# Kernel optimization log

Measured on AMD Instinct MI355X. Metric: run time of the kernel, lower is better.

Reference implementation:

```python
import jax, jax.numpy as jnp
import numpy as np

LAMBDA = 0.7
RATIO = 3
EPS = 1e-6


def setup_inputs() -> dict:
    key = jax.random.key(0)
    k1, k2, k3 = jax.random.split(key, 3)
    bs, n, w, h = 8, 7, 640, 640
    preds = jax.random.normal(k1, (bs, n, w, h), dtype=jnp.float32)
    labels = jax.random.randint(k2, (bs, n, w, h), 0, 2, dtype=jnp.int32)
    training_mask = jax.random.randint(k3, (bs, w, h), 0, 2, dtype=jnp.int32)
    return {"preds": preds, "labels": labels, "training_mask": training_mask}


def _dice(S, G):
    # S, G: [C, P]; per-channel dice coefficient, then mean over channels
    num = 2.0 * jnp.sum(S * G, axis=-1)
    den = jnp.sum(S * S, axis=-1) + jnp.sum(G * G, axis=-1) + EPS
    return jnp.mean(num / den)


def _single_sample(pred, label, mask):
    # pred, label: [n, P]; mask: [P]
    P = pred.shape[-1]
    p = jax.nn.sigmoid(pred)
    pred_n = p[-1] * mask            # masked full-text prediction
    label_n = label[-1] * mask

    # --- OHEM mask M (cal_M): keep all positives + top (ratio*n_pos) hardest negatives ---
    pos = pred_n >= 0.5
    n_pos = jnp.sum(pos)
    n_neg_all = jnp.sum(~pos)
    k = n_pos * RATIO
    # sigmoid outputs are in (0,1); sentinel -1 pushes positives to the end of the descending sort
    neg_vals = jnp.where(pos, -1.0, pred_n)
    sorted_desc = -jnp.sort(-neg_vals)
    thr = sorted_desc[jnp.clip(k - 1, 0, P - 1)]  # k-th largest negative score
    ohem_active = (n_neg_all > k) & (k > 0)
    M = jnp.where(ohem_active, (pred_n >= thr).astype(jnp.float32), 1.0)

    # L_c: dice loss on OHEM-selected full-text map
    L_c = 1.0 - _dice((pred_n * M)[None, :], (label_n * M)[None, :])

    # L_s: dice loss on shrunk kernels, gated by predicted text region W
    W = (pred_n >= 0.5).astype(jnp.float32)
    L_s = 1.0 - _dice(p[:-1] * W, label[:-1] * W)

    loss = LAMBDA * L_c + (1.0 - LAMBDA) * L_s
    return L_c, L_s, loss


def reference(preds, labels, training_mask):
    bs, n, w, h = preds.shape
    preds = preds.reshape(bs, n, w * h)
    labels = labels.reshape(bs, n, w * h).astype(jnp.float32)
    mask = training_mask.reshape(bs, w * h).astype(jnp.float32)
    L_c, L_s, loss = jax.vmap(_single_sample)(preds, labels, mask)
    # reduction='mean'
    return L_c.mean(), L_s.mean(), loss.mean()
```

## Files before the change

### kernel.cpp

```cpp
#include <hip/hip_runtime.h>

#define BS   8
#define NCH  7
#define PX   409600
#define NBIN 65536
#define NCHK 256
#define WIN_LO 0x3000u
#define WIN_SZ 4096
#define EPSF 1e-6f

__device__ __forceinline__ float sigf(float x) {
    return 1.0f / (1.0f + __expf(-x));
}

__device__ __forceinline__ unsigned wred_u(unsigned v) {
    #pragma unroll
    for (int o = 32; o; o >>= 1) v += __shfl_down(v, o);
    return v;
}

__device__ __forceinline__ float wred_f(float v) {
    #pragma unroll
    for (int o = 32; o; o >>= 1) v += __shfl_down(v, o);
    return v;
}

__global__ __launch_bounds__(256) void k_main(const float* __restrict__ preds,
                                              const int* __restrict__ labels,
                                              const int* __restrict__ mask,
                                              unsigned* __restrict__ hist1,
                                              unsigned* __restrict__ chunks1,
                                              unsigned* __restrict__ n_pos,
                                              float* __restrict__ sums) {
    int b = blockIdx.y;
    const float* pr = preds + (size_t)b * NCH * PX;
    const int*   lb = labels + (size_t)b * NCH * PX;
    const int*   mk = mask + (size_t)b * PX;

    __shared__ unsigned lh[WIN_SZ];
    for (int j = threadIdx.x; j < WIN_SZ; j += 256) lh[j] = 0u;
    __syncthreads();

    unsigned pos_cnt = 0, zero_cnt = 0;
    float acc[18];
    #pragma unroll
    for (int j = 0; j < 18; j++) acc[j] = 0.f;

    for (int g = blockIdx.x * 256 + threadIdx.x; g < PX / 4; g += gridDim.x * 256) {
        int px = g * 4;
        float4 p6 = *(const float4*)(pr + 6 * PX + px);
        int4   m4 = *(const int4*)(mk + px);
        float mm[4]  = {(float)m4.x, (float)m4.y, (float)m4.z, (float)m4.w};
        float p6a[4] = {p6.x, p6.y, p6.z, p6.w};
        float W[4];
        #pragma unroll
        for (int u = 0; u < 4; u++) {
            float pn = sigf(p6a[u]) * mm[u];
            if (pn >= 0.5f) {
                pos_cnt++; W[u] = 1.0f;
            } else {
                W[u] = 0.0f;
                unsigned bits = __float_as_uint(pn);
                if (bits == 0u) {
                    zero_cnt++;
                } else {
                    unsigned hb = bits >> 16;
                    if (hb - WIN_LO < WIN_SZ) {
                        atomicAdd(&lh[hb - WIN_LO], 1u);
                    } else {
                        atomicAdd(&hist1[(size_t)b * NBIN + hb], 1u);
                        atomicAdd(&chunks1[b * NCHK + (hb >> 8)], 1u);
                    }
                }
            }
        }
        #pragma unroll
        for (int c = 0; c < 6; c++) {
            float4 pc4 = *(const float4*)(pr + c * PX + px);
            int4   lc4 = *(const int4*)(lb + c * PX + px);
            float pcs[4] = {pc4.x, pc4.y, pc4.z, pc4.w};
            float lcs[4] = {(float)lc4.x, (float)lc4.y, (float)lc4.z, (float)lc4.w};
            #pragma unroll
            for (int u = 0; u < 4; u++) {
                float s = sigf(pcs[u]);
                float l = lcs[u];
                acc[c]      += s * l * W[u];
                acc[6 + c]  += s * s * W[u];
                acc[12 + c] += l * W[u];
            }
        }
    }
    __syncthreads();

    for (int j = threadIdx.x; j < WIN_SZ; j += 256) {
        unsigned c = lh[j];
        if (c) atomicAdd(&hist1[(size_t)b * NBIN + WIN_LO + j], c);
    }
    __shared__ unsigned csum[256];
    {
        unsigned s = 0;
        int chunk = threadIdx.x >> 4, part = threadIdx.x & 15;
        const unsigned* base = &lh[chunk * 256 + part * 16];
        #pragma unroll
        for (int j = 0; j < 16; j++) s += base[j];
        csum[threadIdx.x] = s;
    }
    __syncthreads();
    if (threadIdx.x < 16) {
        unsigned s = 0;
        #pragma unroll
        for (int j = 0; j < 16; j++) s += csum[threadIdx.x * 16 + j];
        if (s) atomicAdd(&chunks1[b * NCHK + 48 + threadIdx.x], s);
    }

    __shared__ unsigned ws2[2][4];
    unsigned pv = wred_u(pos_cnt), zv = wred_u(zero_cnt);
    int lane = threadIdx.x & 63, wid = threadIdx.x >> 6;
    if (lane == 0) { ws2[0][wid] = pv; ws2[1][wid] = zv; }
    __syncthreads();
    if (threadIdx.x == 0) {
        unsigned pt = 0, zt = 0;
        #pragma unroll
        for (int w = 0; w < 4; w++) { pt += ws2[0][w]; zt += ws2[1][w]; }
        if (pt) atomicAdd(&n_pos[b], pt);
        if (zt) {
            atomicAdd(&hist1[(size_t)b * NBIN], zt);
            atomicAdd(&chunks1[b * NCHK], zt);
        }
    }

    __shared__ float red[4][18];
    #pragma unroll
    for (int j = 0; j < 18; j++) {
        float v = wred_f(acc[j]);
        if (lane == 0) red[wid][j] = v;
    }
    __syncthreads();
    if (threadIdx.x < 18) {
        float tot = red[0][threadIdx.x] + red[1][threadIdx.x] +
                    red[2][threadIdx.x] + red[3][threadIdx.x];
        atomicAdd(&sums[b * 21 + 3 + threadIdx.x], tot);
    }
}

__device__ void select2(const unsigned* __restrict__ chunks,
                        const unsigned* __restrict__ bins,
                        unsigned k, unsigned* out_bin, unsigned* out_rank) {
    __shared__ unsigned cs[256];
    __shared__ unsigned sel_c, sel_r;
    int t = threadIdx.x;
    cs[t] = chunks[t];
    __syncthreads();
    #pragma unroll
    for (int off = 1; off < 256; off <<= 1) {
        unsigned v = cs[t];
        unsigned a = (t + off < 256) ? cs[t + off] : 0u;
        __syncthreads();
        cs[t] = v + a;
        __syncthreads();
    }
    {
        unsigned sfx  = cs[t];
        unsigned sfx1 = (t < 255) ? cs[t + 1] : 0u;
        if (sfx >= k && sfx1 < k) { sel_c = (unsigned)t; sel_r = k - sfx1; }
    }
    __syncthreads();
    unsigned chunk = sel_c, krem = sel_r;
    cs[t] = bins[chunk * 256 + t];
    __syncthreads();
    #pragma unroll
    for (int off = 1; off < 256; off <<= 1) {
        unsigned v = cs[t];
        unsigned a = (t + off < 256) ? cs[t + off] : 0u;
        __syncthreads();
        cs[t] = v + a;
        __syncthreads();
    }
    {
        unsigned sfx  = cs[t];
        unsigned sfx1 = (t < 255) ? cs[t + 1] : 0u;
        if (sfx >= krem && sfx1 < krem) {
            *out_bin  = chunk * 256 + (unsigned)t;
            *out_rank = krem - sfx1;
        }
    }
    __syncthreads();
}

__global__ __launch_bounds__(256) void k_find_hi(const unsigned* __restrict__ hist1,
                                                 const unsigned* __restrict__ chunks1,
                                                 const unsigned* __restrict__ n_pos,
                                                 unsigned* __restrict__ hi_bin,
                                                 unsigned* __restrict__ rankv,
                                                 unsigned* __restrict__ activev,
                                                 float* __restrict__ thr) {
    int b = blockIdx.x;
    unsigned np_ = n_pos[b];
    unsigned k = np_ * 3u;
    unsigned nneg = (unsigned)PX - np_;
    if (!(nneg > k && k > 0u)) {
        if (threadIdx.x == 0) { activev[b] = 0u; thr[b] = -1.0f; }
        return;
    }
    __shared__ unsigned rb, rr;
    select2(chunks1 + b * NCHK, hist1 + (size_t)b * NBIN, k, &rb, &rr);
    if (threadIdx.x == 0) {
        activev[b] = 1u;
        hi_bin[b] = rb;
        rankv[b] = rr;
        if (rb == 0u) thr[b] = 0.0f;
    }
}

__global__ __launch_bounds__(256) void k_refine(const float* __restrict__ preds,
                                                const int* __restrict__ mask,
                                                const unsigned* __restrict__ hi_bin,
                                                const unsigned* __restrict__ activev,
                                                unsigned* __restrict__ hist2,
                                                unsigned* __restrict__ chunks2) {
    int b = blockIdx.y;
    if (!activev[b]) return;
    unsigned hi = hi_bin[b];
    if (hi == 0u) return;
    const float* pr = preds + ((size_t)b * NCH + 6) * PX;
    const int* mk = mask + (size_t)b * PX;
    unsigned* h2 = hist2 + (size_t)b * NBIN;
    unsigned* c2 = chunks2 + b * NCHK;
    for (int g = blockIdx.x * 256 + threadIdx.x; g < PX / 4; g += gridDim.x * 256) {
        int px = g * 4;
        float4 p6 = *(const float4*)(pr + px);
        int4   m4 = *(const int4*)(mk + px);
        float p6a[4] = {p6.x, p6.y, p6.z, p6.w};
        float mm[4]  = {(float)m4.x, (float)m4.y, (float)m4.z, (float)m4.w};
        #pragma unroll
        for (int u = 0; u < 4; u++) {
            float pn = sigf(p6a[u]) * mm[u];
            if (pn < 0.5f) {
                unsigned bits = __float_as_uint(pn);
                if ((bits >> 16) == hi) {
                    unsigned lo = bits & 0xFFFFu;
                    atomicAdd(&h2[lo], 1u);
                    atomicAdd(&c2[lo >> 8], 1u);
                }
            }
        }
    }
}

__global__ __launch_bounds__(256) void k_find_lo(const unsigned* __restrict__ hist2,
                                                 const unsigned* __restrict__ chunks2,
                                                 const unsigned* __restrict__ hi_bin,
                                                 const unsigned* __restrict__ rankv,
                                                 const unsigned* __restrict__ activev,
                                                 float* __restrict__ thr) {
    int b = blockIdx.x;
    if (!activev[b]) return;
    unsigned hi = hi_bin[b];
    if (hi == 0u) return;
    __shared__ unsigned rb, rr;
    select2(chunks2 + b * NCHK, hist2 + (size_t)b * NBIN, rankv[b], &rb, &rr);
    if (threadIdx.x == 0) thr[b] = __uint_as_float((hi << 16) | rb);
}

__global__ __launch_bounds__(256) void k_lc(const float* __restrict__ preds,
                                            const int* __restrict__ labels,
                                            const int* __restrict__ mask,
                                            const float* __restrict__ thr,
                                            float* __restrict__ sums) {
    int b = blockIdx.y;
    const float* pr = preds + ((size_t)b * NCH + 6) * PX;
    const int*   lb = labels + ((size_t)b * NCH + 6) * PX;
    const int*   mk = mask + (size_t)b * PX;
    float thr_b = thr[b];

    float a0 = 0.f, a1 = 0.f, a2 = 0.f;
    for (int g = blockIdx.x * 256 + threadIdx.x; g < PX / 4; g += gridDim.x * 256) {
        int px = g * 4;
        float4 p6 = *(const float4*)(pr + px);
        int4   l4 = *(const int4*)(lb + px);
        int4   m4 = *(const int4*)(mk + px);
        float p6a[4] = {p6.x, p6.y, p6.z, p6.w};
        float la[4]  = {(float)l4.x, (float)l4.y, (float)l4.z, (float)l4.w};
        float mm[4]  = {(float)m4.x, (float)m4.y, (float)m4.z, (float)m4.w};
        #pragma unroll
        for (int u = 0; u < 4; u++) {
            float pn = sigf(p6a[u]) * mm[u];
            float Mi = (pn >= thr_b) ? 1.0f : 0.0f;
            float ln = la[u] * mm[u];
            a0 += pn * ln * Mi;
            a1 += pn * pn * Mi;
            a2 += ln * Mi;
        }
    }
    __shared__ float red[4][3];
    int lane = threadIdx.x & 63, wid = threadIdx.x >> 6;
    float v0 = wred_f(a0), v1 = wred_f(a1), v2 = wred_f(a2);
    if (lane == 0) { red[wid][0] = v0; red[wid][1] = v1; red[wid][2] = v2; }
    __syncthreads();
    if (threadIdx.x < 3) {
        float tot = red[0][threadIdx.x] + red[1][threadIdx.x] +
                    red[2][threadIdx.x] + red[3][threadIdx.x];
        atomicAdd(&sums[b * 21 + threadIdx.x], tot);
    }
}

__global__ void k_final(const float* __restrict__ sums, float* __restrict__ out) {
    int t = threadIdx.x;
    float Lc = 0.f, Ls = 0.f;
    if (t < BS) {
        const float* s = sums + t * 21;
        Lc = 1.0f - (2.0f * s[0]) / (s[1] + s[2] + EPSF);
        float acc = 0.f;
        #pragma unroll
        for (int c = 0; c < 6; c++)
            acc += (2.0f * s[3 + c]) / (s[9 + c] + s[15 + c] + EPSF);
        Ls = 1.0f - acc * (1.0f / 6.0f);
    }
    #pragma unroll
    for (int o = 4; o; o >>= 1) { Lc += __shfl_down(Lc, o); Ls += __shfl_down(Ls, o); }
    if (t == 0) {
        float lc_m = Lc * (1.0f / (float)BS);
        float ls_m = Ls * (1.0f / (float)BS);
        out[0] = lc_m;
        out[1] = ls_m;
        out[2] = 0.7f * lc_m + 0.3f * ls_m;
    }
}

extern "C" void kernel_launch(void* const* d_in, const int* in_sizes, int n_in,
                              void* d_out, int out_size, void* d_ws, size_t ws_size,
                              hipStream_t stream) {
    const float* preds = (const float*)d_in[0];
    const int* labels  = (const int*)d_in[1];
    const int* mask    = (const int*)d_in[2];
    float* out = (float*)d_out;

    unsigned* hist1   = (unsigned*)d_ws;
    unsigned* hist2   = hist1 + (size_t)BS * NBIN;
    unsigned* chunks1 = hist2 + (size_t)BS * NBIN;
    unsigned* chunks2 = chunks1 + (size_t)BS * NCHK;
    unsigned* n_pos   = chunks2 + (size_t)BS * NCHK;
    unsigned* hi_bin  = n_pos + BS;
    unsigned* rankv   = hi_bin + BS;
    unsigned* activev = rankv + BS;
    float*    thr     = (float*)(activev + BS);
    float*    sums    = thr + BS;

    size_t zero_words = (size_t)2 * BS * NBIN + (size_t)2 * BS * NCHK + 5 * BS + (size_t)BS * 21;
    hipMemsetAsync(d_ws, 0, zero_words * sizeof(unsigned), stream);

    hipLaunchKernelGGL(k_main, dim3(100, BS), dim3(256), 0, stream,
                       preds, labels, mask, hist1, chunks1, n_pos, sums);

    hipLaunchKernelGGL(k_find_hi, dim3(BS), dim3(256), 0, stream,
                       hist1, chunks1, n_pos, hi_bin, rankv, activev, thr);

    hipLaunchKernelGGL(k_refine, dim3(32, BS), dim3(256), 0, stream,
                       preds, mask, hi_bin, activev, hist2, chunks2);

    hipLaunchKernelGGL(k_find_lo, dim3(BS), dim3(256), 0, stream,
                       hist2, chunks2, hi_bin, rankv, activev, thr);

    hipLaunchKernelGGL(k_lc, dim3(100, BS), dim3(256), 0, stream,
                       preds, labels, mask, thr, sums);

    hipLaunchKernelGGL(k_final, dim3(1), dim3(64), 0, stream, sums, out);
}
```

Measured before the change: 233.0 us.

## Use one-pass-per-thread grids, drop shared window histogram and chunk counters

The main, refine and Lc kernels now launch 400 blocks per sample so each thread handles exactly one float4 group with all loads issued up front, replacing the grid-stride loops over 100 or 32 blocks. The shared-memory window histogram and the separate chunk-count arrays are removed. Every non-positive value goes straight to a global histogram atomic, and select2 now builds its chunk sums by reducing the histogram itself. Float atomics on the sums are replaced by per-block partial writes that k_final reduces, which shrinks the memset. The changes target latency hiding and bookkeeping overhead, but they add heavy global atomic contention on hot histogram bins, since many values fall into a few bins.

```diff
diff --git a/kernel.cpp b/kernel.cpp
--- a/kernel.cpp
+++ b/kernel.cpp
@@ -4,9 +4,7 @@
 #define NCH  7
 #define PX   409600
 #define NBIN 65536
-#define NCHK 256
-#define WIN_LO 0x3000u
-#define WIN_SZ 4096
+#define NBLK 400
 #define EPSF 1e-6f
 
 __device__ __forceinline__ float sigf(float x) {
@@ -25,131 +23,100 @@
     return v;
 }
 
-__global__ __launch_bounds__(256) void k_main(const float* __restrict__ preds,
-                                              const int* __restrict__ labels,
-                                              const int* __restrict__ mask,
-                                              unsigned* __restrict__ hist1,
-                                              unsigned* __restrict__ chunks1,
-                                              unsigned* __restrict__ n_pos,
-                                              float* __restrict__ sums) {
+__global__ __launch_bounds__(256, 4) void k_main(const float* __restrict__ preds,
+                                                 const int* __restrict__ labels,
+                                                 const int* __restrict__ mask,
+                                                 unsigned* __restrict__ hist1,
+                                                 unsigned* __restrict__ n_pos,
+                                                 float* __restrict__ part) {
     int b = blockIdx.y;
+    int bx = blockIdx.x;
+    int px = (bx * 256 + threadIdx.x) * 4;
     const float* pr = preds + (size_t)b * NCH * PX;
     const int*   lb = labels + (size_t)b * NCH * PX;
     const int*   mk = mask + (size_t)b * PX;
 
-    __shared__ unsigned lh[WIN_SZ];
-    for (int j = threadIdx.x; j < WIN_SZ; j += 256) lh[j] = 0u;
-    __syncthreads();
-
+    float4 p6 = *(const float4*)(pr + 6 * PX + px);
+    int4   m4 = *(const int4*)(mk + px);
+    float4 pc[6];
+    int4   lc[6];
+    #pragma unroll
+    for (int c = 0; c < 6; c++) {
+        pc[c] = *(const float4*)(pr + c * PX + px);
+        lc[c] = *(const int4*)(lb + c * PX + px);
+    }
+
+    float mm[4]  = {(float)m4.x, (float)m4.y, (float)m4.z, (float)m4.w};
+    float p6a[4] = {p6.x, p6.y, p6.z, p6.w};
+    float W[4];
     unsigned pos_cnt = 0, zero_cnt = 0;
+    unsigned* hb = hist1 + (size_t)b * NBIN;
+
+    #pragma unroll
+    for (int u = 0; u < 4; u++) {
+        float pn = sigf(p6a[u]) * mm[u];
+        if (pn >= 0.5f) {
+            pos_cnt++; W[u] = 1.0f;
+        } else {
+            W[u] = 0.0f;
+            unsigned bits = __float_as_uint(pn);
+            if (bits == 0u) zero_cnt++;
+            else            atomicAdd(&hb[bits >> 16], 1u);
+        }
+    }
+
     float acc[18];
     #pragma unroll
     for (int j = 0; j < 18; j++) acc[j] = 0.f;
-
-    for (int g = blockIdx.x * 256 + threadIdx.x; g < PX / 4; g += gridDim.x * 256) {
-        int px = g * 4;
-        float4 p6 = *(const float4*)(pr + 6 * PX + px);
-        int4   m4 = *(const int4*)(mk + px);
-        float mm[4]  = {(float)m4.x, (float)m4.y, (float)m4.z, (float)m4.w};
-        float p6a[4] = {p6.x, p6.y, p6.z, p6.w};
-        float W[4];
+    #pragma unroll
+    for (int c = 0; c < 6; c++) {
+        float pcs[4] = {pc[c].x, pc[c].y, pc[c].z, pc[c].w};
+        float lcs[4] = {(float)lc[c].x, (float)lc[c].y, (float)lc[c].z, (float)lc[c].w};
         #pragma unroll
         for (int u = 0; u < 4; u++) {
-            float pn = sigf(p6a[u]) * mm[u];
-            if (pn >= 0.5f) {
-                pos_cnt++; W[u] = 1.0f;
-            } else {
-                W[u] = 0.0f;
-                unsigned bits = __float_as_uint(pn);
-                if (bits == 0u) {
-                    zero_cnt++;
-                } else {
-                    unsigned hb = bits >> 16;
-                    if (hb - WIN_LO < WIN_SZ) {
-                        atomicAdd(&lh[hb - WIN_LO], 1u);
-                    } else {
-                        atomicAdd(&hist1[(size_t)b * NBIN + hb], 1u);
-                        atomicAdd(&chunks1[b * NCHK + (hb >> 8)], 1u);
-                    }
-                }
-            }
-        }
-        #pragma unroll
-        for (int c = 0; c < 6; c++) {
-            float4 pc4 = *(const float4*)(pr + c * PX + px);
-            int4   lc4 = *(const int4*)(lb + c * PX + px);
-            float pcs[4] = {pc4.x, pc4.y, pc4.z, pc4.w};
-            float lcs[4] = {(float)lc4.x, (float)lc4.y, (float)lc4.z, (float)lc4.w};
-            #pragma unroll
-            for (int u = 0; u < 4; u++) {
-                float s = sigf(pcs[u]);
-                float l = lcs[u];
-                acc[c]      += s * l * W[u];
-                acc[6 + c]  += s * s * W[u];
-                acc[12 + c] += l * W[u];
-            }
-        }
-    }
-    __syncthreads();
-
-    for (int j = threadIdx.x; j < WIN_SZ; j += 256) {
-        unsigned c = lh[j];
-        if (c) atomicAdd(&hist1[(size_t)b * NBIN + WIN_LO + j], c);
-    }
-    __shared__ unsigned csum[256];
-    {
-        unsigned s = 0;
-        int chunk = threadIdx.x >> 4, part = threadIdx.x & 15;
-        const unsigned* base = &lh[chunk * 256 + part * 16];
-        #pragma unroll
-        for (int j = 0; j < 16; j++) s += base[j];
-        csum[threadIdx.x] = s;
-    }
-    __syncthreads();
-    if (threadIdx.x < 16) {
-        unsigned s = 0;
-        #pragma unroll
-        for (int j = 0; j < 16; j++) s += csum[threadIdx.x * 16 + j];
-        if (s) atomicAdd(&chunks1[b * NCHK + 48 + threadIdx.x], s);
-    }
-
+            float s = sigf(pcs[u]);
+            float l = lcs[u];
+            acc[c]      += s * l * W[u];
+            acc[6 + c]  += s * s * W[u];
+            acc[12 + c] += l * W[u];
+        }
+    }
+
+    int lane = threadIdx.x & 63, wid = threadIdx.x >> 6;
+    __shared__ float red[4][18];
     __shared__ unsigned ws2[2][4];
-    unsigned pv = wred_u(pos_cnt), zv = wred_u(zero_cnt);
-    int lane = threadIdx.x & 63, wid = threadIdx.x >> 6;
-    if (lane == 0) { ws2[0][wid] = pv; ws2[1][wid] = zv; }
-    __syncthreads();
-    if (threadIdx.x == 0) {
-        unsigned pt = 0, zt = 0;
-        #pragma unroll
-        for (int w = 0; w < 4; w++) { pt += ws2[0][w]; zt += ws2[1][w]; }
-        if (pt) atomicAdd(&n_pos[b], pt);
-        if (zt) {
-            atomicAdd(&hist1[(size_t)b * NBIN], zt);
-            atomicAdd(&chunks1[b * NCHK], zt);
-        }
-    }
-
-    __shared__ float red[4][18];
     #pragma unroll
     for (int j = 0; j < 18; j++) {
         float v = wred_f(acc[j]);
         if (lane == 0) red[wid][j] = v;
     }
+    unsigned pv = wred_u(pos_cnt), zv = wred_u(zero_cnt);
+    if (lane == 0) { ws2[0][wid] = pv; ws2[1][wid] = zv; }
     __syncthreads();
     if (threadIdx.x < 18) {
         float tot = red[0][threadIdx.x] + red[1][threadIdx.x] +
                     red[2][threadIdx.x] + red[3][threadIdx.x];
-        atomicAdd(&sums[b * 21 + 3 + threadIdx.x], tot);
-    }
-}
-
-__device__ void select2(const unsigned* __restrict__ chunks,
-                        const unsigned* __restrict__ bins,
-                        unsigned k, unsigned* out_bin, unsigned* out_rank) {
+        part[((size_t)b * 21 + 3 + threadIdx.x) * NBLK + bx] = tot;
+    }
+    if (threadIdx.x == 0) {
+        unsigned pt = ws2[0][0] + ws2[0][1] + ws2[0][2] + ws2[0][3];
+        unsigned zt = ws2[1][0] + ws2[1][1] + ws2[1][2] + ws2[1][3];
+        if (pt) atomicAdd(&n_pos[b], pt);
+        if (zt) atomicAdd(&hb[0], zt);
+    }
+}
+
+__device__ void select2(const unsigned* __restrict__ bins, unsigned k,
+                        unsigned* out_bin, unsigned* out_rank) {
     __shared__ unsigned cs[256];
     __shared__ unsigned sel_c, sel_r;
-    int t = threadIdx.x;
-    cs[t] = chunks[t];
+    int t = threadIdx.x, lane = t & 63, wid = t >> 6;
+
+    for (int c = wid * 64; c < wid * 64 + 64; c++) {
+        uint4 v = *((const uint4*)(bins + c * 256) + lane);
+        unsigned s = wred_u(v.x + v.y + v.z + v.w);
+        if (lane == 0) cs[c] = s;
+    }
     __syncthreads();
     #pragma unroll
     for (int off = 1; off < 256; off <<= 1) {
@@ -188,7 +155,6 @@
 }
 
 __global__ __launch_bounds__(256) void k_find_hi(const unsigned* __restrict__ hist1,
-                                                 const unsigned* __restrict__ chunks1,
                                                  const unsigned* __restrict__ n_pos,
                                                  unsigned* __restrict__ hi_bin,
                                                  unsigned* __restrict__ rankv,
@@ -203,7 +169,7 @@
         return;
     }
     __shared__ unsigned rb, rr;
-    select2(chunks1 + b * NCHK, hist1 + (size_t)b * NBIN, k, &rb, &rr);
+    select2(hist1 + (size_t)b * NBIN, k, &rb, &rr);
     if (threadIdx.x == 0) {
         activev[b] = 1u;
         hi_bin[b] = rb;
@@ -216,39 +182,30 @@
                                                 const int* __restrict__ mask,
                                                 const unsigned* __restrict__ hi_bin,
                                                 const unsigned* __restrict__ activev,
-                                                unsigned* __restrict__ hist2,
-                                                unsigned* __restrict__ chunks2) {
+                                                unsigned* __restrict__ hist2) {
     int b = blockIdx.y;
     if (!activev[b]) return;
     unsigned hi = hi_bin[b];
     if (hi == 0u) return;
+    int px = (blockIdx.x * 256 + threadIdx.x) * 4;
     const float* pr = preds + ((size_t)b * NCH + 6) * PX;
     const int* mk = mask + (size_t)b * PX;
     unsigned* h2 = hist2 + (size_t)b * NBIN;
-    unsigned* c2 = chunks2 + b * NCHK;
-    for (int g = blockIdx.x * 256 + threadIdx.x; g < PX / 4; g += gridDim.x * 256) {
-        int px = g * 4;
-        float4 p6 = *(const float4*)(pr + px);
-        int4   m4 = *(const int4*)(mk + px);
-        float p6a[4] = {p6.x, p6.y, p6.z, p6.w};
-        float mm[4]  = {(float)m4.x, (float)m4.y, (float)m4.z, (float)m4.w};
-        #pragma unroll
-        for (int u = 0; u < 4; u++) {
-            float pn = sigf(p6a[u]) * mm[u];
-            if (pn < 0.5f) {
-                unsigned bits = __float_as_uint(pn);
-                if ((bits >> 16) == hi) {
-                    unsigned lo = bits & 0xFFFFu;
-                    atomicAdd(&h2[lo], 1u);
-                    atomicAdd(&c2[lo >> 8], 1u);
-                }
-            }
+    float4 p6 = *(const float4*)(pr + px);
+    int4   m4 = *(const int4*)(mk + px);
+    float p6a[4] = {p6.x, p6.y, p6.z, p6.w};
+    float mm[4]  = {(float)m4.x, (float)m4.y, (float)m4.z, (float)m4.w};
+    #pragma unroll
+    for (int u = 0; u < 4; u++) {
+        float pn = sigf(p6a[u]) * mm[u];
+        if (pn < 0.5f) {
+            unsigned bits = __float_as_uint(pn);
+            if ((bits >> 16) == hi) atomicAdd(&h2[bits & 0xFFFFu], 1u);
         }
     }
 }
 
 __global__ __launch_bounds__(256) void k_find_lo(const unsigned* __restrict__ hist2,
-                                                 const unsigned* __restrict__ chunks2,
                                                  const unsigned* __restrict__ hi_bin,
                                                  const unsigned* __restrict__ rankv,
                                                  const unsigned* __restrict__ activev,
@@ -258,39 +215,39 @@
     unsigned hi = hi_bin[b];
     if (hi == 0u) return;
     __shared__ unsigned rb, rr;
-    select2(chunks2 + b * NCHK, hist2 + (size_t)b * NBIN, rankv[b], &rb, &rr);
+    select2(hist2 + (size_t)b * NBIN, rankv[b], &rb, &rr);
     if (threadIdx.x == 0) thr[b] = __uint_as_float((hi << 16) | rb);
 }
 
-__global__ __launch_bounds__(256) void k_lc(const float* __restrict__ preds,
-                                            const int* __restrict__ labels,
-                                            const int* __restrict__ mask,
-                                            const float* __restrict__ thr,
-                                            float* __restrict__ sums) {
+__global__ __launch_bounds__(256, 4) void k_lc(const float* __restrict__ preds,
+                                               const int* __restrict__ labels,
+                                               const int* __restrict__ mask,
+                                               const float* __restrict__ thr,
+                                               float* __restrict__ part) {
     int b = blockIdx.y;
+    int bx = blockIdx.x;
+    int px = (bx * 256 + threadIdx.x) * 4;
     const float* pr = preds + ((size_t)b * NCH + 6) * PX;
     const int*   lb = labels + ((size_t)b * NCH + 6) * PX;
     const int*   mk = mask + (size_t)b * PX;
     float thr_b = thr[b];
 
+    float4 p6 = *(const float4*)(pr + px);
+    int4   l4 = *(const int4*)(lb + px);
+    int4   m4 = *(const int4*)(mk + px);
+    float p6a[4] = {p6.x, p6.y, p6.z, p6.w};
+    float la[4]  = {(float)l4.x, (float)l4.y, (float)l4.z, (float)l4.w};
+    float mm[4]  = {(float)m4.x, (float)m4.y, (float)m4.z, (float)m4.w};
+
     float a0 = 0.f, a1 = 0.f, a2 = 0.f;
-    for (int g = blockIdx.x * 256 + threadIdx.x; g < PX / 4; g += gridDim.x * 256) {
-        int px = g * 4;
-        float4 p6 = *(const float4*)(pr + px);
-        int4   l4 = *(const int4*)(lb + px);
-        int4   m4 = *(const int4*)(mk + px);
-        float p6a[4] = {p6.x, p6.y, p6.z, p6.w};
-        float la[4]  = {(float)l4.x, (float)l4.y, (float)l4.z, (float)l4.w};
-        float mm[4]  = {(float)m4.x, (float)m4.y, (float)m4.z, (float)m4.w};
-        #pragma unroll
-        for (int u = 0; u < 4; u++) {
-            float pn = sigf(p6a[u]) * mm[u];
-            float Mi = (pn >= thr_b) ? 1.0f : 0.0f;
-            float ln = la[u] * mm[u];
-            a0 += pn * ln * Mi;
-            a1 += pn * pn * Mi;
-            a2 += ln * Mi;
-        }
+    #pragma unroll
+    for (int u = 0; u < 4; u++) {
+        float pn = sigf(p6a[u]) * mm[u];
+        float Mi = (pn >= thr_b) ? 1.0f : 0.0f;
+        float ln = la[u] * mm[u];
+        a0 += pn * ln * Mi;
+        a1 += pn * pn * Mi;
+        a2 += ln * Mi;
     }
     __shared__ float red[4][3];
     int lane = threadIdx.x & 63, wid = threadIdx.x >> 6;
@@ -300,25 +257,34 @@
     if (threadIdx.x < 3) {
         float tot = red[0][threadIdx.x] + red[1][threadIdx.x] +
                     red[2][threadIdx.x] + red[3][threadIdx.x];
-        atomicAdd(&sums[b * 21 + threadIdx.x], tot);
-    }
-}
-
-__global__ void k_final(const float* __restrict__ sums, float* __restrict__ out) {
-    int t = threadIdx.x;
-    float Lc = 0.f, Ls = 0.f;
-    if (t < BS) {
-        const float* s = sums + t * 21;
-        Lc = 1.0f - (2.0f * s[0]) / (s[1] + s[2] + EPSF);
-        float acc = 0.f;
+        part[((size_t)b * 21 + threadIdx.x) * NBLK + bx] = tot;
+    }
+}
+
+__global__ __launch_bounds__(256) void k_final(const float* __restrict__ part,
+                                               float* __restrict__ out) {
+    __shared__ float fr[BS * 21];
+    int lane = threadIdx.x & 63, wid = threadIdx.x >> 6;
+    for (int r = wid; r < BS * 21; r += 4) {
+        const float* row = part + (size_t)r * NBLK;
+        float s = 0.f;
+        for (int c = lane; c < NBLK; c += 64) s += row[c];
+        s = wred_f(s);
+        if (lane == 0) fr[r] = s;
+    }
+    __syncthreads();
+    if (threadIdx.x == 0) {
+        float Lc = 0.f, Ls = 0.f;
         #pragma unroll
-        for (int c = 0; c < 6; c++)
-            acc += (2.0f * s[3 + c]) / (s[9 + c] + s[15 + c] + EPSF);
-        Ls = 1.0f - acc * (1.0f / 6.0f);
-    }
-    #pragma unroll
-    for (int o = 4; o; o >>= 1) { Lc += __shfl_down(Lc, o); Ls += __shfl_down(Ls, o); }
-    if (t == 0) {
+        for (int b = 0; b < BS; b++) {
+            const float* s = fr + b * 21;
+            Lc += 1.0f - (2.0f * s[0]) / (s[1] + s[2] + EPSF);
+            float acc = 0.f;
+            #pragma unroll
+            for (int c = 0; c < 6; c++)
+                acc += (2.0f * s[3 + c]) / (s[9 + c] + s[15 + c] + EPSF);
+            Ls += 1.0f - acc * (1.0f / 6.0f);
+        }
         float lc_m = Lc * (1.0f / (float)BS);
         float ls_m = Ls * (1.0f / (float)BS);
         out[0] = lc_m;
@@ -337,32 +303,30 @@
 
     unsigned* hist1   = (unsigned*)d_ws;
     unsigned* hist2   = hist1 + (size_t)BS * NBIN;
-    unsigned* chunks1 = hist2 + (size_t)BS * NBIN;
-    unsigned* chunks2 = chunks1 + (size_t)BS * NCHK;
-    unsigned* n_pos   = chunks2 + (size_t)BS * NCHK;
+    unsigned* n_pos   = hist2 + (size_t)BS * NBIN;
     unsigned* hi_bin  = n_pos + BS;
     unsigned* rankv   = hi_bin + BS;
     unsigned* activev = rankv + BS;
     float*    thr     = (float*)(activev + BS);
-    float*    sums    = thr + BS;
-
-    size_t zero_words = (size_t)2 * BS * NBIN + (size_t)2 * BS * NCHK + 5 * BS + (size_t)BS * 21;
+    float*    part    = thr + BS;
+
+    size_t zero_words = (size_t)2 * BS * NBIN + BS;
     hipMemsetAsync(d_ws, 0, zero_words * sizeof(unsigned), stream);
 
-    hipLaunchKernelGGL(k_main, dim3(100, BS), dim3(256), 0, stream,
-                       preds, labels, mask, hist1, chunks1, n_pos, sums);
+    hipLaunchKernelGGL(k_main, dim3(NBLK, BS), dim3(256), 0, stream,
+                       preds, labels, mask, hist1, n_pos, part);
 
     hipLaunchKernelGGL(k_find_hi, dim3(BS), dim3(256), 0, stream,
-                       hist1, chunks1, n_pos, hi_bin, rankv, activev, thr);
-
-    hipLaunchKernelGGL(k_refine, dim3(32, BS), dim3(256), 0, stream,
-                       preds, mask, hi_bin, activev, hist2, chunks2);
+                       hist1, n_pos, hi_bin, rankv, activev, thr);
+
+    hipLaunchKernelGGL(k_refine, dim3(NBLK, BS), dim3(256), 0, stream,
+                       preds, mask, hi_bin, activev, hist2);
 
     hipLaunchKernelGGL(k_find_lo, dim3(BS), dim3(256), 0, stream,
-                       hist2, chunks2, hi_bin, rankv, activev, thr);
-
-    hipLaunchKernelGGL(k_lc, dim3(100, BS), dim3(256), 0, stream,
-                       preds, labels, mask, thr, sums);
-
-    hipLaunchKernelGGL(k_final, dim3(1), dim3(64), 0, stream, sums, out);
-}
+                       hist2, hi_bin, rankv, activev, thr);
+
+    hipLaunchKernelGGL(k_lc, dim3(NBLK, BS), dim3(256), 0, stream,
+                       preds, labels, mask, thr, part);
+
+    hipLaunchKernelGGL(k_final, dim3(1), dim3(256), 0, stream, part, out);
+}
```

Measured after the change: 512.6 us. +120.0%, slower.
